# Kernel tuning notes

Measured on AMD Instinct MI355X. Metric: run time of the kernel, lower is better.

## Reference

```python
import jax, jax.numpy as jnp
import numpy as np

N_HEADS = 16  # matches init_kwargs

def setup_inputs() -> dict:
    key = jax.random.key(0)
    kq, kk, kv = jax.random.split(key, 3)
    B, L, S, D = 4, 2048, 2048, 1024
    queries = jax.random.normal(kq, (B, L, D), dtype=jnp.float32)
    keys = jax.random.normal(kk, (B, S, D), dtype=jnp.float32)
    values = jax.random.normal(kv, (B, S, D), dtype=jnp.float32)
    # TriangularCausalMask: True above the diagonal (positions to mask)
    causal = jnp.triu(jnp.ones((L, S), dtype=bool), k=1)
    attn_mask = jnp.broadcast_to(causal[None, None], (B, 1, L, S))
    return {"queries": queries, "keys": keys, "values": values, "attn_mask": attn_mask}

def reference(queries, keys, values, attn_mask):
    B, L, _ = queries.shape
    S = keys.shape[1]
    H = N_HEADS
    q = queries.reshape(B, L, H, -1)   # (B,L,H,E)
    k = keys.reshape(B, S, H, -1)      # (B,S,H,E)
    v = values.reshape(B, S, H, -1)    # (B,S,H,E)
    scale = 1.0 / jnp.sqrt(jnp.asarray(q.shape[-1], dtype=q.dtype))
    scores = jnp.einsum('blhe,bshe->bhls', q, k)          # (B,H,L,S)
    scores = jnp.where(attn_mask, -jnp.inf, scores)        # masked_fill_
    A = jax.nn.softmax(scale * scores, axis=-1)            # dropout is identity (p=0 / eval)
    V = jnp.einsum('bhls,bshd->blhd', A, v)                # (B,L,H,E)
    return V.reshape(B, L, -1)
```

## Files before the change

kernel.cpp:

```cpp
#include <hip/hip_runtime.h>
#include <hip/hip_bf16.h>

typedef __attribute__((ext_vector_type(8))) short short8;
typedef __attribute__((ext_vector_type(4))) short short4v;
typedef __attribute__((ext_vector_type(4))) float floatx4;

constexpr int B = 4, L = 2048, H = 16, E = 64, D = 1024;
constexpr int QT = 128, KT = 64;
constexpr int STR = 72;
constexpr float SCL_LOG2E = 0.125f * 1.4426950408889634f;

__device__ __forceinline__ short bf16_bits(float x) {
    __hip_bfloat16 b = __float2bfloat16(x);
    return *(const short*)&b;
}

__device__ __forceinline__ short8 packq8(float4 a, float4 c, float scl) {
    short8 r;
    r[0] = bf16_bits(a.x * scl); r[1] = bf16_bits(a.y * scl);
    r[2] = bf16_bits(a.z * scl); r[3] = bf16_bits(a.w * scl);
    r[4] = bf16_bits(c.x * scl); r[5] = bf16_bits(c.y * scl);
    r[6] = bf16_bits(c.z * scl); r[7] = bf16_bits(c.w * scl);
    return r;
}

__global__ __launch_bounds__(256)
void prep_kv(const float* __restrict__ K, const float* __restrict__ V,
             short* __restrict__ Kb, short* __restrict__ Vt)
{
    __shared__ __align__(16) short vt[64 * STR];
    const int tid = threadIdx.x;
    const int bh = blockIdx.x >> 5, kt = blockIdx.x & 31;
    const int b = bh >> 4, h = bh & 15;

    const float* Kp = K + ((size_t)(b * L + kt * 64)) * D + h * E;
    const float* Vp = V + ((size_t)(b * L + kt * 64)) * D + h * E;
    short* Kop = Kb + ((size_t)(bh * 32 + kt)) * 4096;
    short* Vop = Vt + ((size_t)(bh * 32 + kt)) * 4096;

    #pragma unroll
    for (int it = 0; it < 2; ++it) {
        int f = it * 256 + tid;
        int nt = f >> 7, hh = (f >> 6) & 1, qd = (f >> 4) & 3, cc = f & 15;
        int s = nt * 16 + cc, d0 = hh * 32 + qd * 8;
        const float* p = Kp + (size_t)s * D + d0;
        float4 x = *(const float4*)p;
        float4 y = *(const float4*)(p + 4);
        union { short sh[8]; uint4 u; } pk;
        pk.sh[0] = bf16_bits(x.x); pk.sh[1] = bf16_bits(x.y);
        pk.sh[2] = bf16_bits(x.z); pk.sh[3] = bf16_bits(x.w);
        pk.sh[4] = bf16_bits(y.x); pk.sh[5] = bf16_bits(y.y);
        pk.sh[6] = bf16_bits(y.z); pk.sh[7] = bf16_bits(y.w);
        *(uint4*)(Kop + (size_t)f * 8) = pk.u;
    }

    #pragma unroll
    for (int p = 0; p < 4; ++p) {
        int idx = p * 256 + tid;
        int s = idx >> 4, c4 = (idx & 15) * 4;
        float4 g = *(const float4*)(Vp + (size_t)s * D + c4);
        vt[(c4 + 0) * STR + s] = bf16_bits(g.x);
        vt[(c4 + 1) * STR + s] = bf16_bits(g.y);
        vt[(c4 + 2) * STR + s] = bf16_bits(g.z);
        vt[(c4 + 3) * STR + s] = bf16_bits(g.w);
    }
    __syncthreads();

    #pragma unroll
    for (int it = 0; it < 2; ++it) {
        int f16 = it * 256 + tid;
        int f8 = f16 * 2;
        int st = f8 >> 8, dt = (f8 >> 6) & 3, qd = (f8 >> 4) & 3;
        int cA = f8 & 15;
        int dA = dt * 16 + cA, dB = dA + 1;
        int s0 = st * 16 + qd * 4;
        uint2 a = *(const uint2*)&vt[dA * STR + s0];
        uint2 c = *(const uint2*)&vt[dB * STR + s0];
        uint4 u; u.x = a.x; u.y = a.y; u.z = c.x; u.w = c.y;
        *(uint4*)(Vop + (size_t)f16 * 8) = u;
    }
}

__global__ __launch_bounds__(512, 4)
void attn_fwd_p(const float* __restrict__ Q, const short* __restrict__ Kb,
                const short* __restrict__ Vt, float* __restrict__ O)
{
    __shared__ __align__(16) short k_s[2 * 4096];
    __shared__ __align__(16) short v_s[2 * 4096];

    const int tid  = threadIdx.x;
    const int wave = tid >> 6;
    const int lane = tid & 63;
    const int c16  = lane & 15;
    const int quad = lane >> 4;

    const int i  = (int)blockIdx.x;
    const int bh = ((i >> 6) << 3) | (i & 7);
    const int pr = (i >> 3) & 7;
    const int b  = bh >> 4;
    const int h  = bh & 15;

    const float* Qp  = Q  + ((size_t)b * L) * D + h * E;
    const short* Kbp = Kb + ((size_t)bh * 32) * 4096;
    const short* Vtp = Vt + ((size_t)bh * 32) * 4096;
    float*       Op  = O  + ((size_t)b * L) * D + h * E;

    for (int sub = 0; sub < 2; ++sub) {
        const int qt = (sub == 0) ? (15 - pr) : pr;
        const int q_base = qt * QT;
        const int n_tiles = 2 * qt + 2;
        const int m0 = q_base + wave * 16;

        const float* qrow = Qp + (size_t)(q_base + wave * 16 + c16) * D + quad * 8;
        short8 qf0 = packq8(*(const float4*)(qrow),      *(const float4*)(qrow + 4),  SCL_LOG2E);
        short8 qf1 = packq8(*(const float4*)(qrow + 32), *(const float4*)(qrow + 36), SCL_LOG2E);

        uint4 kr = *(const uint4*)(Kbp + (size_t)tid * 8);
        uint4 vr = *(const uint4*)(Vtp + (size_t)tid * 8);
        __syncthreads();
        *(uint4*)&k_s[tid * 8] = kr;
        *(uint4*)&v_s[tid * 8] = vr;

        floatx4 o[4];
        #pragma unroll
        for (int dt = 0; dt < 4; ++dt) o[dt] = (floatx4){0.f, 0.f, 0.f, 0.f};
        float lsum = 0.f;

        for (int t = 0; t < n_tiles; ++t) {
            __syncthreads();
            const short* kc = k_s + (t & 1) * 4096;
            const short* vc = v_s + (t & 1) * 4096;
            short* kn = k_s + ((t + 1) & 1) * 4096;
            short* vn = v_s + ((t + 1) & 1) * 4096;

            const bool more = (t + 1 < n_tiles);
            if (more) {
                const size_t nb = (size_t)(t + 1) * 4096 + (size_t)tid * 8;
                kr = *(const uint4*)(Kbp + nb);
                vr = *(const uint4*)(Vtp + nb);
            }

            if (t * 64 <= m0 + 15) {
                const bool diag = (t * 64 + 63 > m0);
                short4v pa[4];
                #pragma unroll
                for (int nt = 0; nt < 4; ++nt) {
                    short8 kb0 = *(const short8*)&kc[nt * 1024 + lane * 8];
                    short8 kb1 = *(const short8*)&kc[nt * 1024 + 512 + lane * 8];
                    floatx4 acc = (floatx4){0.f, 0.f, 0.f, 0.f};
                    acc = __builtin_amdgcn_mfma_f32_16x16x32_bf16(kb0, qf0, acc, 0, 0, 0);
                    acc = __builtin_amdgcn_mfma_f32_16x16x32_bf16(kb1, qf1, acc, 0, 0, 0);
                    if (diag) {
                        const int s0 = t * 64 + nt * 16 + quad * 4;
                        const int m  = m0 + c16;
                        #pragma unroll
                        for (int r = 0; r < 4; ++r)
                            if (s0 + r > m) acc[r] = -__builtin_inff();
                    }
                    #pragma unroll
                    for (int r = 0; r < 4; ++r) {
                        float p = exp2f(acc[r]);
                        lsum += p;
                        pa[nt][r] = bf16_bits(p);
                    }
                }
                #pragma unroll
                for (int st = 0; st < 4; ++st) {
                    #pragma unroll
                    for (int dt = 0; dt < 4; ++dt) {
                        short4v vb = *(const short4v*)&vc[(st * 4 + dt) * 256 + lane * 4];
                        o[dt] = __builtin_amdgcn_mfma_f32_16x16x16bf16_1k(pa[st], vb, o[dt], 0, 0, 0);
                    }
                }
            }

            if (more) {
                *(uint4*)&kn[tid * 8] = kr;
                *(uint4*)&vn[tid * 8] = vr;
            }
        }

        lsum += __shfl_xor(lsum, 16);
        lsum += __shfl_xor(lsum, 32);
        const int row0 = q_base + wave * 16 + quad * 4;
        #pragma unroll
        for (int r = 0; r < 4; ++r) {
            const float inv = 1.f / __shfl(lsum, quad * 4 + r);
            #pragma unroll
            for (int dt = 0; dt < 4; ++dt)
                Op[(size_t)(row0 + r) * D + dt * 16 + c16] = o[dt][r] * inv;
        }
    }
}

__global__ __launch_bounds__(256, 2)
void attn_fwd_fb(const float* __restrict__ Q, const float* __restrict__ K,
                 const float* __restrict__ V, float* __restrict__ O)
{
    constexpr int FSTR = 72;
    constexpr int FQT = 64;
    __shared__ __align__(16) short q_s[FQT * FSTR];
    __shared__ __align__(16) short k_s[64 * FSTR];
    __shared__ __align__(16) short vt_s[E * FSTR];
    __shared__ __align__(16) short p_s[4][16 * FSTR];

    const int tid  = threadIdx.x;
    const int wave = tid >> 6;
    const int lane = tid & 63;
    const int c16  = lane & 15;
    const int quad = lane >> 4;

    const int nqt = L / FQT;
    const int qt  = (nqt - 1) - (int)(blockIdx.x % nqt);
    const int bh  = blockIdx.x / nqt;
    const int b   = bh >> 4;
    const int h   = bh & 15;
    const int q_base = qt * FQT;

    const float* Qp = Q + ((size_t)b * L) * D + h * E;
    const float* Kp = K + ((size_t)b * L) * D + h * E;
    const float* Vp = V + ((size_t)b * L) * D + h * E;
    float*       Op = O + ((size_t)b * L) * D + h * E;

    #pragma unroll
    for (int p = 0; p < 4; ++p) {
        int idx = p * 256 + tid;
        int r = idx >> 4, c4 = (idx & 15) * 4;
        float4 f = *(const float4*)(Qp + (size_t)(q_base + r) * D + c4);
        union { short s[4]; uint2 u; } pk;
        pk.s[0] = bf16_bits(f.x); pk.s[1] = bf16_bits(f.y);
        pk.s[2] = bf16_bits(f.z); pk.s[3] = bf16_bits(f.w);
        *(uint2*)&q_s[r * FSTR + c4] = pk.u;
    }
    __syncthreads();

    short8 qf0 = *(const short8*)&q_s[(wave * 16 + c16) * FSTR + quad * 8];
    short8 qf1 = *(const short8*)&q_s[(wave * 16 + c16) * FSTR + 32 + quad * 8];

    floatx4 o_acc[4];
    #pragma unroll
    for (int nt = 0; nt < 4; ++nt) o_acc[nt] = (floatx4){0.f, 0.f, 0.f, 0.f};
    float m_run[4], l_run[4];
    #pragma unroll
    for (int r = 0; r < 4; ++r) { m_run[r] = -__builtin_inff(); l_run[r] = 0.f; }

    for (int t = 0; t <= qt; ++t) {
        const int k_base = t * 64;
        __syncthreads();
        #pragma unroll
        for (int p = 0; p < 4; ++p) {
            int idx = p * 256 + tid;
            int r = idx >> 4, c4 = (idx & 15) * 4;
            float4 f = *(const float4*)(Kp + (size_t)(k_base + r) * D + c4);
            union { short s[4]; uint2 u; } pk;
            pk.s[0] = bf16_bits(f.x); pk.s[1] = bf16_bits(f.y);
            pk.s[2] = bf16_bits(f.z); pk.s[3] = bf16_bits(f.w);
            *(uint2*)&k_s[r * FSTR + c4] = pk.u;
        }
        #pragma unroll
        for (int p = 0; p < 4; ++p) {
            int s  = lane;
            int dg = p * 4 + wave;
            float4 f = *(const float4*)(Vp + (size_t)(k_base + s) * D + dg * 4);
            vt_s[(dg * 4 + 0) * FSTR + s] = bf16_bits(f.x);
            vt_s[(dg * 4 + 1) * FSTR + s] = bf16_bits(f.y);
            vt_s[(dg * 4 + 2) * FSTR + s] = bf16_bits(f.z);
            vt_s[(dg * 4 + 3) * FSTR + s] = bf16_bits(f.w);
        }
        __syncthreads();

        floatx4 sc[4];
        #pragma unroll
        for (int nt = 0; nt < 4; ++nt) {
            floatx4 acc = (floatx4){0.f, 0.f, 0.f, 0.f};
            short8 b0 = *(const short8*)&k_s[(nt * 16 + c16) * FSTR + quad * 8];
            short8 b1 = *(const short8*)&k_s[(nt * 16 + c16) * FSTR + 32 + quad * 8];
            acc = __builtin_amdgcn_mfma_f32_16x16x32_bf16(qf0, b0, acc, 0, 0, 0);
            acc = __builtin_amdgcn_mfma_f32_16x16x32_bf16(qf1, b1, acc, 0, 0, 0);
            sc[nt] = acc;
        }

        const int q_row0 = q_base + wave * 16 + quad * 4;
        #pragma unroll
        for (int nt = 0; nt < 4; ++nt) {
            const int k_col = k_base + nt * 16 + c16;
            #pragma unroll
            for (int r = 0; r < 4; ++r) {
                float s = sc[nt][r] * SCL_LOG2E;
                sc[nt][r] = (k_col <= q_row0 + r) ? s : -__builtin_inff();
            }
        }

        float alpha[4];
        #pragma unroll
        for (int r = 0; r < 4; ++r) {
            float mx = fmaxf(fmaxf(sc[0][r], sc[1][r]), fmaxf(sc[2][r], sc[3][r]));
            mx = fmaxf(mx, __shfl_xor(mx, 1));
            mx = fmaxf(mx, __shfl_xor(mx, 2));
            mx = fmaxf(mx, __shfl_xor(mx, 4));
            mx = fmaxf(mx, __shfl_xor(mx, 8));
            const float m_new = fmaxf(m_run[r], mx);
            alpha[r] = exp2f(m_run[r] - m_new);
            m_run[r] = m_new;
        }
        float psum[4] = {0.f, 0.f, 0.f, 0.f};
        #pragma unroll
        for (int nt = 0; nt < 4; ++nt) {
            #pragma unroll
            for (int r = 0; r < 4; ++r) {
                float p = exp2f(sc[nt][r] - m_run[r]);
                sc[nt][r] = p;
                psum[r] += p;
            }
        }
        #pragma unroll
        for (int r = 0; r < 4; ++r) {
            float s = psum[r];
            s += __shfl_xor(s, 1);
            s += __shfl_xor(s, 2);
            s += __shfl_xor(s, 4);
            s += __shfl_xor(s, 8);
            l_run[r] = l_run[r] * alpha[r] + s;
            #pragma unroll
            for (int nt = 0; nt < 4; ++nt) o_acc[nt][r] *= alpha[r];
        }

        short* pw = &p_s[wave][0];
        #pragma unroll
        for (int nt = 0; nt < 4; ++nt) {
            #pragma unroll
            for (int r = 0; r < 4; ++r)
                pw[(quad * 4 + r) * FSTR + nt * 16 + c16] = bf16_bits(sc[nt][r]);
        }
        __syncthreads();

        #pragma unroll
        for (int kc = 0; kc < 2; ++kc) {
            short8 pa = *(const short8*)&pw[c16 * FSTR + kc * 32 + quad * 8];
            #pragma unroll
            for (int nt = 0; nt < 4; ++nt) {
                short8 vb = *(const short8*)&vt_s[(nt * 16 + c16) * FSTR + kc * 32 + quad * 8];
                o_acc[nt] = __builtin_amdgcn_mfma_f32_16x16x32_bf16(pa, vb, o_acc[nt], 0, 0, 0);
            }
        }
    }

    const int q_row0 = q_base + wave * 16 + quad * 4;
    #pragma unroll
    for (int r = 0; r < 4; ++r) {
        const float inv_l = 1.f / l_run[r];
        #pragma unroll
        for (int nt = 0; nt < 4; ++nt)
            Op[(size_t)(q_row0 + r) * D + nt * 16 + c16] = o_acc[nt][r] * inv_l;
    }
}

extern "C" void kernel_launch(void* const* d_in, const int* in_sizes, int n_in,
                              void* d_out, int out_size, void* d_ws, size_t ws_size,
                              hipStream_t stream)
{
    const float* Q = (const float*)d_in[0];
    const float* K = (const float*)d_in[1];
    const float* V = (const float*)d_in[2];
    float* O = (float*)d_out;

    const size_t elems = (size_t)B * H * L * E;
    const size_t need  = 2 * elems * sizeof(short);

    if (ws_size >= need) {
        short* Kb = (short*)d_ws;
        short* Vt = Kb + elems;
        prep_kv<<<dim3(B * H * 32), dim3(256), 0, stream>>>(K, V, Kb, Vt);
        attn_fwd_p<<<dim3(B * H * 8), dim3(512), 0, stream>>>(Q, Kb, Vt, O);
    } else {
        attn_fwd_fb<<<dim3(B * H * (L / 64)), dim3(256), 0, stream>>>(Q, K, V, O);
    }
}
```

Before: 223.9 us.

## Process both paired query tiles in one K/V sweep with direct-to-LDS loads

Instead of two sequential passes over K/V for the paired query tiles (15-pr and pr), each block now holds both Q fragments and accumulators and streams K/V tiles once, feeding each tile to both query groups. K/V staging uses global_load_lds so data goes straight from global memory into LDS without a register round trip. Diagonal tiles skip fully masked 16-column sub-blocks, and the MFMA section runs at raised wave priority. In exchange, register pressure rises from the doubled accumulators, and correctness depends on the direct LDS loads completing before the barrier.

```diff
diff --git a/kernel.cpp b/kernel.cpp
--- a/kernel.cpp
+++ b/kernel.cpp
@@ -6,7 +6,6 @@
 typedef __attribute__((ext_vector_type(4))) float floatx4;
 
 constexpr int B = 4, L = 2048, H = 16, E = 64, D = 1024;
-constexpr int QT = 128, KT = 64;
 constexpr int STR = 72;
 constexpr float SCL_LOG2E = 0.125f * 1.4426950408889634f;
 
@@ -22,6 +21,12 @@
     r[4] = bf16_bits(c.x * scl); r[5] = bf16_bits(c.y * scl);
     r[6] = bf16_bits(c.z * scl); r[7] = bf16_bits(c.w * scl);
     return r;
+}
+
+__device__ __forceinline__ void load_lds16(const short* g, short* l) {
+    __builtin_amdgcn_global_load_lds(
+        (const __attribute__((address_space(1))) unsigned int*)g,
+        (__attribute__((address_space(3))) unsigned int*)l, 16, 0, 0);
 }
 
 __global__ __launch_bounds__(256)
@@ -81,6 +86,86 @@
     }
 }
 
+__device__ __forceinline__ void frag_step(
+    const short* __restrict__ kc, const short* __restrict__ vc,
+    short8 qf0, short8 qf1, int m0, int t,
+    floatx4 (&o)[4], float& lsum, int c16, int quad, int lane)
+{
+    short4v pa[4];
+    const int rel = m0 + 15 - t * 64;
+    if (rel >= 78) {
+        #pragma unroll
+        for (int nt = 0; nt < 4; ++nt) {
+            short8 kb0 = *(const short8*)&kc[nt * 1024 + lane * 8];
+            short8 kb1 = *(const short8*)&kc[nt * 1024 + 512 + lane * 8];
+            floatx4 acc = (floatx4){0.f, 0.f, 0.f, 0.f};
+            acc = __builtin_amdgcn_mfma_f32_16x16x32_bf16(kb0, qf0, acc, 0, 0, 0);
+            acc = __builtin_amdgcn_mfma_f32_16x16x32_bf16(kb1, qf1, acc, 0, 0, 0);
+            #pragma unroll
+            for (int r = 0; r < 4; ++r) {
+                float p = exp2f(acc[r]);
+                lsum += p;
+                pa[nt][r] = bf16_bits(p);
+            }
+        }
+        #pragma unroll
+        for (int st = 0; st < 4; ++st) {
+            #pragma unroll
+            for (int dt = 0; dt < 4; ++dt) {
+                short4v vb = *(const short4v*)&vc[(st * 4 + dt) * 256 + lane * 4];
+                o[dt] = __builtin_amdgcn_mfma_f32_16x16x16bf16_1k(pa[st], vb, o[dt], 0, 0, 0);
+            }
+        }
+    } else {
+        const int cnt = (rel >> 4) >= 3 ? 4 : ((rel >> 4) + 1);
+        const int m = m0 + c16;
+        #pragma unroll
+        for (int nt = 0; nt < 4; ++nt) {
+            if (nt < cnt) {
+                short8 kb0 = *(const short8*)&kc[nt * 1024 + lane * 8];
+                short8 kb1 = *(const short8*)&kc[nt * 1024 + 512 + lane * 8];
+                floatx4 acc = (floatx4){0.f, 0.f, 0.f, 0.f};
+                acc = __builtin_amdgcn_mfma_f32_16x16x32_bf16(kb0, qf0, acc, 0, 0, 0);
+                acc = __builtin_amdgcn_mfma_f32_16x16x32_bf16(kb1, qf1, acc, 0, 0, 0);
+                const int s0 = t * 64 + nt * 16 + quad * 4;
+                #pragma unroll
+                for (int r = 0; r < 4; ++r) {
+                    if (s0 + r > m) acc[r] = -__builtin_inff();
+                    float p = exp2f(acc[r]);
+                    lsum += p;
+                    pa[nt][r] = bf16_bits(p);
+                }
+            }
+        }
+        #pragma unroll
+        for (int st = 0; st < 4; ++st) {
+            if (st < cnt) {
+                #pragma unroll
+                for (int dt = 0; dt < 4; ++dt) {
+                    short4v vb = *(const short4v*)&vc[(st * 4 + dt) * 256 + lane * 4];
+                    o[dt] = __builtin_amdgcn_mfma_f32_16x16x16bf16_1k(pa[st], vb, o[dt], 0, 0, 0);
+                }
+            }
+        }
+    }
+}
+
+__device__ __forceinline__ void store_frag(
+    float lsum, const floatx4 (&o)[4], float* __restrict__ Op,
+    int row_base, int c16, int quad)
+{
+    lsum += __shfl_xor(lsum, 16);
+    lsum += __shfl_xor(lsum, 32);
+    const int row0 = row_base + quad * 4;
+    #pragma unroll
+    for (int r = 0; r < 4; ++r) {
+        const float inv = 1.f / __shfl(lsum, quad * 4 + r);
+        #pragma unroll
+        for (int dt = 0; dt < 4; ++dt)
+            Op[(size_t)(row0 + r) * D + dt * 16 + c16] = o[dt][r] * inv;
+    }
+}
+
 __global__ __launch_bounds__(512, 4)
 void attn_fwd_p(const float* __restrict__ Q, const short* __restrict__ Kb,
                 const short* __restrict__ Vt, float* __restrict__ O)
@@ -105,92 +190,52 @@
     const short* Vtp = Vt + ((size_t)bh * 32) * 4096;
     float*       Op  = O  + ((size_t)b * L) * D + h * E;
 
-    for (int sub = 0; sub < 2; ++sub) {
-        const int qt = (sub == 0) ? (15 - pr) : pr;
-        const int q_base = qt * QT;
-        const int n_tiles = 2 * qt + 2;
-        const int m0 = q_base + wave * 16;
-
-        const float* qrow = Qp + (size_t)(q_base + wave * 16 + c16) * D + quad * 8;
-        short8 qf0 = packq8(*(const float4*)(qrow),      *(const float4*)(qrow + 4),  SCL_LOG2E);
-        short8 qf1 = packq8(*(const float4*)(qrow + 32), *(const float4*)(qrow + 36), SCL_LOG2E);
-
-        uint4 kr = *(const uint4*)(Kbp + (size_t)tid * 8);
-        uint4 vr = *(const uint4*)(Vtp + (size_t)tid * 8);
+    const int qtA = 15 - pr, qtB = pr;
+    const int nA  = 2 * qtA + 2;
+    const int mA  = qtA * 128 + wave * 16;
+    const int mB  = qtB * 128 + wave * 16;
+
+    const float* qra = Qp + (size_t)(mA + c16) * D + quad * 8;
+    short8 qfA0 = packq8(*(const float4*)(qra),      *(const float4*)(qra + 4),  SCL_LOG2E);
+    short8 qfA1 = packq8(*(const float4*)(qra + 32), *(const float4*)(qra + 36), SCL_LOG2E);
+    const float* qrb = Qp + (size_t)(mB + c16) * D + quad * 8;
+    short8 qfB0 = packq8(*(const float4*)(qrb),      *(const float4*)(qrb + 4),  SCL_LOG2E);
+    short8 qfB1 = packq8(*(const float4*)(qrb + 32), *(const float4*)(qrb + 36), SCL_LOG2E);
+
+    load_lds16(Kbp + (size_t)tid * 8, k_s + wave * 512);
+    load_lds16(Vtp + (size_t)tid * 8, v_s + wave * 512);
+
+    floatx4 oA[4], oB[4];
+    #pragma unroll
+    for (int dt = 0; dt < 4; ++dt) {
+        oA[dt] = (floatx4){0.f, 0.f, 0.f, 0.f};
+        oB[dt] = (floatx4){0.f, 0.f, 0.f, 0.f};
+    }
+    float lA = 0.f, lB = 0.f;
+
+    for (int t = 0; t < nA; ++t) {
         __syncthreads();
-        *(uint4*)&k_s[tid * 8] = kr;
-        *(uint4*)&v_s[tid * 8] = vr;
-
-        floatx4 o[4];
-        #pragma unroll
-        for (int dt = 0; dt < 4; ++dt) o[dt] = (floatx4){0.f, 0.f, 0.f, 0.f};
-        float lsum = 0.f;
-
-        for (int t = 0; t < n_tiles; ++t) {
-            __syncthreads();
-            const short* kc = k_s + (t & 1) * 4096;
-            const short* vc = v_s + (t & 1) * 4096;
-            short* kn = k_s + ((t + 1) & 1) * 4096;
-            short* vn = v_s + ((t + 1) & 1) * 4096;
-
-            const bool more = (t + 1 < n_tiles);
-            if (more) {
-                const size_t nb = (size_t)(t + 1) * 4096 + (size_t)tid * 8;
-                kr = *(const uint4*)(Kbp + nb);
-                vr = *(const uint4*)(Vtp + nb);
-            }
-
-            if (t * 64 <= m0 + 15) {
-                const bool diag = (t * 64 + 63 > m0);
-                short4v pa[4];
-                #pragma unroll
-                for (int nt = 0; nt < 4; ++nt) {
-                    short8 kb0 = *(const short8*)&kc[nt * 1024 + lane * 8];
-                    short8 kb1 = *(const short8*)&kc[nt * 1024 + 512 + lane * 8];
-                    floatx4 acc = (floatx4){0.f, 0.f, 0.f, 0.f};
-                    acc = __builtin_amdgcn_mfma_f32_16x16x32_bf16(kb0, qf0, acc, 0, 0, 0);
-                    acc = __builtin_amdgcn_mfma_f32_16x16x32_bf16(kb1, qf1, acc, 0, 0, 0);
-                    if (diag) {
-                        const int s0 = t * 64 + nt * 16 + quad * 4;
-                        const int m  = m0 + c16;
-                        #pragma unroll
-                        for (int r = 0; r < 4; ++r)
-                            if (s0 + r > m) acc[r] = -__builtin_inff();
-                    }
-                    #pragma unroll
-                    for (int r = 0; r < 4; ++r) {
-                        float p = exp2f(acc[r]);
-                        lsum += p;
-                        pa[nt][r] = bf16_bits(p);
-                    }
-                }
-                #pragma unroll
-                for (int st = 0; st < 4; ++st) {
-                    #pragma unroll
-                    for (int dt = 0; dt < 4; ++dt) {
-                        short4v vb = *(const short4v*)&vc[(st * 4 + dt) * 256 + lane * 4];
-                        o[dt] = __builtin_amdgcn_mfma_f32_16x16x16bf16_1k(pa[st], vb, o[dt], 0, 0, 0);
-                    }
-                }
-            }
-
-            if (more) {
-                *(uint4*)&kn[tid * 8] = kr;
-                *(uint4*)&vn[tid * 8] = vr;
-            }
-        }
-
-        lsum += __shfl_xor(lsum, 16);
-        lsum += __shfl_xor(lsum, 32);
-        const int row0 = q_base + wave * 16 + quad * 4;
-        #pragma unroll
-        for (int r = 0; r < 4; ++r) {
-            const float inv = 1.f / __shfl(lsum, quad * 4 + r);
-            #pragma unroll
-            for (int dt = 0; dt < 4; ++dt)
-                Op[(size_t)(row0 + r) * D + dt * 16 + c16] = o[dt][r] * inv;
-        }
-    }
+        const short* kc = k_s + (t & 1) * 4096;
+        const short* vc = v_s + (t & 1) * 4096;
+
+        if (t + 1 < nA) {
+            const size_t nb = (size_t)(t + 1) * 4096 + (size_t)tid * 8;
+            short* kn = k_s + ((t + 1) & 1) * 4096 + wave * 512;
+            short* vn = v_s + ((t + 1) & 1) * 4096 + wave * 512;
+            load_lds16(Kbp + nb, kn);
+            load_lds16(Vtp + nb, vn);
+        }
+
+        __builtin_amdgcn_s_setprio(1);
+        if (t * 64 <= mA + 15)
+            frag_step(kc, vc, qfA0, qfA1, mA, t, oA, lA, c16, quad, lane);
+        if (t * 64 <= mB + 15)
+            frag_step(kc, vc, qfB0, qfB1, mB, t, oB, lB, c16, quad, lane);
+        __builtin_amdgcn_s_setprio(0);
+    }
+
+    store_frag(lA, oA, Op, mA, c16, quad);
+    store_frag(lB, oB, Op, mB, c16, quad);
 }
 
 __global__ __launch_bounds__(256, 2)
```

New measurement: 227.6 us. About the same (+1.7%).

## Restructure attention into single-wave blocks streaming K/V tiles from global into registers

Applied to the files above, without the earlier changes.

Replaces the 512-thread block with shared-memory double buffering by one-wave blocks. Each block owns a 64-row query tile as four 16-row fragments and streams K/V tiles from global memory into registers, prefetching one tile ahead, so no LDS or barriers are needed. The V layout produced by the prep kernel changes so P·V can use the 16x16x32 MFMA. Masking now uses a per-lane threshold with exp2 zeroing only on diagonal tiles, and s_setprio raises priority around compute. This trades LDS traffic and sync for higher register pressure and repeated global/L2 reads of K/V across blocks, with a new query-tile ordering meant to balance the causal workload.

```diff
diff --git a/kernel.cpp b/kernel.cpp
--- a/kernel.cpp
+++ b/kernel.cpp
@@ -6,7 +6,6 @@
 typedef __attribute__((ext_vector_type(4))) float floatx4;
 
 constexpr int B = 4, L = 2048, H = 16, E = 64, D = 1024;
-constexpr int QT = 128, KT = 64;
 constexpr int STR = 72;
 constexpr float SCL_LOG2E = 0.125f * 1.4426950408889634f;
 
@@ -22,6 +21,17 @@
     r[4] = bf16_bits(c.x * scl); r[5] = bf16_bits(c.y * scl);
     r[6] = bf16_bits(c.z * scl); r[7] = bf16_bits(c.w * scl);
     return r;
+}
+
+__device__ __forceinline__ short8 cat4(short4v a, short4v b) {
+    short8 r;
+    r[0] = a[0]; r[1] = a[1]; r[2] = a[2]; r[3] = a[3];
+    r[4] = b[0]; r[5] = b[1]; r[6] = b[2]; r[7] = b[3];
+    return r;
+}
+
+__device__ __forceinline__ short8 as8(uint4 u) {
+    union { uint4 a; short8 b; } c; c.a = u; return c.b;
 }
 
 __global__ __launch_bounds__(256)
@@ -69,128 +79,185 @@
     #pragma unroll
     for (int it = 0; it < 2; ++it) {
         int f16 = it * 256 + tid;
-        int f8 = f16 * 2;
-        int st = f8 >> 8, dt = (f8 >> 6) & 3, qd = (f8 >> 4) & 3;
-        int cA = f8 & 15;
-        int dA = dt * 16 + cA, dB = dA + 1;
-        int s0 = st * 16 + qd * 4;
-        uint2 a = *(const uint2*)&vt[dA * STR + s0];
-        uint2 c = *(const uint2*)&vt[dB * STR + s0];
-        uint4 u; u.x = a.x; u.y = a.y; u.z = c.x; u.w = c.y;
+        int sp = f16 >> 8, dt = (f16 >> 6) & 3, qd = (f16 >> 4) & 3, cc = f16 & 15;
+        int d = dt * 16 + cc;
+        int s0 = sp * 32 + qd * 4;
+        uint2 lo = *(const uint2*)&vt[d * STR + s0];
+        uint2 hi = *(const uint2*)&vt[d * STR + s0 + 16];
+        uint4 u; u.x = lo.x; u.y = lo.y; u.z = hi.x; u.w = hi.y;
         *(uint4*)(Vop + (size_t)f16 * 8) = u;
     }
 }
 
-__global__ __launch_bounds__(512, 4)
+struct KV { uint4 k[4]; uint4 v[4]; };
+
+__device__ __forceinline__ KV load_tile(const short* __restrict__ Kt,
+                                        const short* __restrict__ Vl, int t)
+{
+    KV r;
+    const short* kp = Kt + (size_t)t * 2048;
+    const short* vp = Vl + (size_t)t * 2048;
+    #pragma unroll
+    for (int j = 0; j < 4; ++j) {
+        r.k[j] = *(const uint4*)(kp + j * 512);
+        r.v[j] = *(const uint4*)(vp + j * 512);
+    }
+    return r;
+}
+
+__device__ __forceinline__ void qkexp(short8 k0, short8 k1, short8 q0, short8 q1,
+                                      float& l, short4v& p)
+{
+    floatx4 a = (floatx4){0.f, 0.f, 0.f, 0.f};
+    a = __builtin_amdgcn_mfma_f32_16x16x32_bf16(k0, q0, a, 0, 0, 0);
+    a = __builtin_amdgcn_mfma_f32_16x16x32_bf16(k1, q1, a, 0, 0, 0);
+    #pragma unroll
+    for (int r = 0; r < 4; ++r) {
+        float e = __builtin_amdgcn_exp2f(a[r]);
+        l += e;
+        p[r] = bf16_bits(e);
+    }
+}
+
+__device__ __forceinline__ void qkexp_diag(short8 k0, short8 k1, short8 q0, short8 q1,
+                                           int thr, float& l, short4v& p)
+{
+    floatx4 a = (floatx4){0.f, 0.f, 0.f, 0.f};
+    a = __builtin_amdgcn_mfma_f32_16x16x32_bf16(k0, q0, a, 0, 0, 0);
+    a = __builtin_amdgcn_mfma_f32_16x16x32_bf16(k1, q1, a, 0, 0, 0);
+    #pragma unroll
+    for (int r = 0; r < 4; ++r) {
+        float e = (r > thr) ? 0.f : __builtin_amdgcn_exp2f(a[r]);
+        l += e;
+        p[r] = bf16_bits(e);
+    }
+}
+
+__device__ __forceinline__ void step_full4(const KV& s, const short8 (&q)[4][2],
+                                           floatx4 (&o)[4][4], float (&l)[4])
+{
+    const short8 k00 = as8(s.k[0]), k01 = as8(s.k[1]);
+    const short8 k10 = as8(s.k[2]), k11 = as8(s.k[3]);
+    #pragma unroll
+    for (int f = 0; f < 4; ++f) {
+        short4v p0, p1;
+        qkexp(k00, k01, q[f][0], q[f][1], l[f], p0);
+        qkexp(k10, k11, q[f][0], q[f][1], l[f], p1);
+        const short8 pa = cat4(p0, p1);
+        #pragma unroll
+        for (int dt = 0; dt < 4; ++dt)
+            o[f][dt] = __builtin_amdgcn_mfma_f32_16x16x32_bf16(pa, as8(s.v[dt]), o[f][dt], 0, 0, 0);
+    }
+}
+
+template<int TAIL>
+__device__ __forceinline__ void step_tail(const KV& s, const short8 (&q)[4][2],
+                                          floatx4 (&o)[4][4], float (&l)[4], int thr)
+{
+    const short8 k00 = as8(s.k[0]), k01 = as8(s.k[1]);
+    const short8 k10 = as8(s.k[2]), k11 = as8(s.k[3]);
+    #pragma unroll
+    for (int f = 0; f < 4; ++f) {
+        const int role = (TAIL == 0) ? ((f == 0) ? 0 : (f == 1) ? 1 : 2)
+                                     : ((f < 2) ? 3 : (f == 2) ? 0 : 1);
+        if (role == 3) continue;
+        short4v p0, p1;
+        if (role == 0) {
+            qkexp_diag(k00, k01, q[f][0], q[f][1], thr, l[f], p0);
+            p1 = (short4v){0, 0, 0, 0};
+        } else if (role == 1) {
+            qkexp(k00, k01, q[f][0], q[f][1], l[f], p0);
+            qkexp_diag(k10, k11, q[f][0], q[f][1], thr, l[f], p1);
+        } else {
+            qkexp(k00, k01, q[f][0], q[f][1], l[f], p0);
+            qkexp(k10, k11, q[f][0], q[f][1], l[f], p1);
+        }
+        const short8 pa = cat4(p0, p1);
+        #pragma unroll
+        for (int dt = 0; dt < 4; ++dt)
+            o[f][dt] = __builtin_amdgcn_mfma_f32_16x16x32_bf16(pa, as8(s.v[dt]), o[f][dt], 0, 0, 0);
+    }
+}
+
+__device__ __forceinline__ void store_frag(
+    float lsum, const floatx4 (&o)[4], float* __restrict__ Op,
+    int row_base, int c16, int quad)
+{
+    lsum += __shfl_xor(lsum, 16);
+    lsum += __shfl_xor(lsum, 32);
+    const int row0 = row_base + quad * 4;
+    #pragma unroll
+    for (int r = 0; r < 4; ++r) {
+        const float inv = 1.f / __shfl(lsum, quad * 4 + r);
+        #pragma unroll
+        for (int dt = 0; dt < 4; ++dt)
+            Op[(size_t)(row0 + r) * D + dt * 16 + c16] = o[dt][r] * inv;
+    }
+}
+
+__global__ __launch_bounds__(64, 2)
 void attn_fwd_p(const float* __restrict__ Q, const short* __restrict__ Kb,
                 const short* __restrict__ Vt, float* __restrict__ O)
 {
-    __shared__ __align__(16) short k_s[2 * 4096];
-    __shared__ __align__(16) short v_s[2 * 4096];
-
-    const int tid  = threadIdx.x;
-    const int wave = tid >> 6;
-    const int lane = tid & 63;
+    const int lane = threadIdx.x;
     const int c16  = lane & 15;
     const int quad = lane >> 4;
 
     const int i  = (int)blockIdx.x;
-    const int bh = ((i >> 6) << 3) | (i & 7);
-    const int pr = (i >> 3) & 7;
+    const int bh = (((i >> 3) & 7) << 3) | (i & 7);
+    const int w  = (i >> 6) & 3;
+    const int u  = (i >> 8) & 7;
+    const int qt = 4 * u + ((u & 1) ? (3 - w) : w);
     const int b  = bh >> 4;
     const int h  = bh & 15;
 
-    const float* Qp  = Q  + ((size_t)b * L) * D + h * E;
-    const short* Kbp = Kb + ((size_t)bh * 32) * 4096;
-    const short* Vtp = Vt + ((size_t)bh * 32) * 4096;
-    float*       Op  = O  + ((size_t)b * L) * D + h * E;
-
-    for (int sub = 0; sub < 2; ++sub) {
-        const int qt = (sub == 0) ? (15 - pr) : pr;
-        const int q_base = qt * QT;
-        const int n_tiles = 2 * qt + 2;
-        const int m0 = q_base + wave * 16;
-
-        const float* qrow = Qp + (size_t)(q_base + wave * 16 + c16) * D + quad * 8;
-        short8 qf0 = packq8(*(const float4*)(qrow),      *(const float4*)(qrow + 4),  SCL_LOG2E);
-        short8 qf1 = packq8(*(const float4*)(qrow + 32), *(const float4*)(qrow + 36), SCL_LOG2E);
-
-        uint4 kr = *(const uint4*)(Kbp + (size_t)tid * 8);
-        uint4 vr = *(const uint4*)(Vtp + (size_t)tid * 8);
-        __syncthreads();
-        *(uint4*)&k_s[tid * 8] = kr;
-        *(uint4*)&v_s[tid * 8] = vr;
-
-        floatx4 o[4];
-        #pragma unroll
-        for (int dt = 0; dt < 4; ++dt) o[dt] = (floatx4){0.f, 0.f, 0.f, 0.f};
-        float lsum = 0.f;
-
-        for (int t = 0; t < n_tiles; ++t) {
-            __syncthreads();
-            const short* kc = k_s + (t & 1) * 4096;
-            const short* vc = v_s + (t & 1) * 4096;
-            short* kn = k_s + ((t + 1) & 1) * 4096;
-            short* vn = v_s + ((t + 1) & 1) * 4096;
-
-            const bool more = (t + 1 < n_tiles);
-            if (more) {
-                const size_t nb = (size_t)(t + 1) * 4096 + (size_t)tid * 8;
-                kr = *(const uint4*)(Kbp + nb);
-                vr = *(const uint4*)(Vtp + nb);
-            }
-
-            if (t * 64 <= m0 + 15) {
-                const bool diag = (t * 64 + 63 > m0);
-                short4v pa[4];
-                #pragma unroll
-                for (int nt = 0; nt < 4; ++nt) {
-                    short8 kb0 = *(const short8*)&kc[nt * 1024 + lane * 8];
-                    short8 kb1 = *(const short8*)&kc[nt * 1024 + 512 + lane * 8];
-                    floatx4 acc = (floatx4){0.f, 0.f, 0.f, 0.f};
-                    acc = __builtin_amdgcn_mfma_f32_16x16x32_bf16(kb0, qf0, acc, 0, 0, 0);
-                    acc = __builtin_amdgcn_mfma_f32_16x16x32_bf16(kb1, qf1, acc, 0, 0, 0);
-                    if (diag) {
-                        const int s0 = t * 64 + nt * 16 + quad * 4;
-                        const int m  = m0 + c16;
-                        #pragma unroll
-                        for (int r = 0; r < 4; ++r)
-                            if (s0 + r > m) acc[r] = -__builtin_inff();
-                    }
-                    #pragma unroll
-                    for (int r = 0; r < 4; ++r) {
-                        float p = exp2f(acc[r]);
-                        lsum += p;
-                        pa[nt][r] = bf16_bits(p);
-                    }
-                }
-                #pragma unroll
-                for (int st = 0; st < 4; ++st) {
-                    #pragma unroll
-                    for (int dt = 0; dt < 4; ++dt) {
-                        short4v vb = *(const short4v*)&vc[(st * 4 + dt) * 256 + lane * 4];
-                        o[dt] = __builtin_amdgcn_mfma_f32_16x16x16bf16_1k(pa[st], vb, o[dt], 0, 0, 0);
-                    }
-                }
-            }
-
-            if (more) {
-                *(uint4*)&kn[tid * 8] = kr;
-                *(uint4*)&vn[tid * 8] = vr;
-            }
-        }
-
-        lsum += __shfl_xor(lsum, 16);
-        lsum += __shfl_xor(lsum, 32);
-        const int row0 = q_base + wave * 16 + quad * 4;
-        #pragma unroll
-        for (int r = 0; r < 4; ++r) {
-            const float inv = 1.f / __shfl(lsum, quad * 4 + r);
-            #pragma unroll
-            for (int dt = 0; dt < 4; ++dt)
-                Op[(size_t)(row0 + r) * D + dt * 16 + c16] = o[dt][r] * inv;
-        }
-    }
+    const float* Qp = Q + ((size_t)b * L) * D + h * E;
+    const short* Kt = Kb + ((size_t)bh * 32) * 4096 + lane * 8;
+    const short* Vl = Vt + ((size_t)bh * 32) * 4096 + lane * 8;
+    float*       Op = O + ((size_t)b * L) * D + h * E;
+
+    const int m0  = qt * 64;
+    const int thr = c16 - quad * 4;
+
+    short8 q[4][2];
+    #pragma unroll
+    for (int f = 0; f < 4; ++f) {
+        const float* qr = Qp + (size_t)(m0 + 16 * f + c16) * D + quad * 8;
+        q[f][0] = packq8(*(const float4*)(qr),      *(const float4*)(qr + 4),  SCL_LOG2E);
+        q[f][1] = packq8(*(const float4*)(qr + 32), *(const float4*)(qr + 36), SCL_LOG2E);
+    }
+
+    floatx4 o[4][4];
+    #pragma unroll
+    for (int f = 0; f < 4; ++f) {
+        #pragma unroll
+        for (int dt = 0; dt < 4; ++dt) o[f][dt] = (floatx4){0.f, 0.f, 0.f, 0.f};
+    }
+    float l[4] = {0.f, 0.f, 0.f, 0.f};
+
+    const int nfull = 2 * qt;
+
+    KV A = load_tile(Kt, Vl, 0);
+    KV Bv;
+    for (int t = 0; t < nfull; t += 2) {
+        Bv = load_tile(Kt, Vl, t + 1);
+        __builtin_amdgcn_s_setprio(1);
+        step_full4(A, q, o, l);
+        __builtin_amdgcn_s_setprio(0);
+        A = load_tile(Kt, Vl, t + 2);
+        __builtin_amdgcn_s_setprio(1);
+        step_full4(Bv, q, o, l);
+        __builtin_amdgcn_s_setprio(0);
+    }
+    Bv = load_tile(Kt, Vl, nfull + 1);
+    __builtin_amdgcn_s_setprio(1);
+    step_tail<0>(A,  q, o, l, thr);
+    step_tail<1>(Bv, q, o, l, thr);
+    __builtin_amdgcn_s_setprio(0);
+
+    #pragma unroll
+    for (int f = 0; f < 4; ++f)
+        store_frag(l[f], o[f], Op, m0 + 16 * f, c16, quad);
 }
 
 __global__ __launch_bounds__(256, 2)
@@ -371,7 +438,7 @@
         short* Kb = (short*)d_ws;
         short* Vt = Kb + elems;
         prep_kv<<<dim3(B * H * 32), dim3(256), 0, stream>>>(K, V, Kb, Vt);
-        attn_fwd_p<<<dim3(B * H * 8), dim3(512), 0, stream>>>(Q, Kb, Vt, O);
+        attn_fwd_p<<<dim3(2048), dim3(64), 0, stream>>>(Q, Kb, Vt, O);
     } else {
         attn_fwd_fb<<<dim3(B * H * (L / 64)), dim3(256), 0, stream>>>(Q, K, V, O);
     }
```

After: 210.6 us, median of 2. -5.9%, faster.
